# Optimization experiments

Hardware: AMD Instinct MI355X
Metric: run time of the kernel (lower is better)

Reference implementation:

```python
import jax, jax.numpy as jnp
import numpy as np

OBS_DIM = 256
FEAT = 128
HID = 64
N_OPT = 8
ACT_N = 18
B = 32768
TEMPERATURE = 1.0


def setup_inputs() -> dict:
    key = jax.random.key(0)
    ks = jax.random.split(key, 16)
    s = 0.05
    inp = {
        "obs": jax.random.normal(ks[0], (B, OBS_DIM), dtype=jnp.float32),
        "act": jax.random.randint(ks[1], (B,), 0, ACT_N, dtype=jnp.int32),
        "opt": jax.random.randint(ks[2], (B,), 0, N_OPT, dtype=jnp.int32),
        # feature trunk: obs_dim -> 64 -> 128, ReLU after both layers
        "fW1": jax.random.normal(ks[3], (HID, OBS_DIM), dtype=jnp.float32) * s,
        "fb1": jnp.zeros((HID,), dtype=jnp.float32),
        "fW2": jax.random.normal(ks[4], (FEAT, HID), dtype=jnp.float32) * s,
        "fb2": jnp.zeros((FEAT,), dtype=jnp.float32),
        # option policy / termination heads: 128 -> n_opts
        "pW": jax.random.normal(ks[5], (N_OPT, FEAT), dtype=jnp.float32) * s,
        "pb": jnp.zeros((N_OPT,), dtype=jnp.float32),
        "tW": jax.random.normal(ks[6], (N_OPT, FEAT), dtype=jnp.float32) * s,
        "tb": jnp.zeros((N_OPT,), dtype=jnp.float32),
        # per-option expert ensemble: 128 -> 64 -> act_n
        "oW1": jax.random.normal(ks[7], (N_OPT, HID, FEAT), dtype=jnp.float32) * s,
        "ob1": jnp.zeros((N_OPT, HID), dtype=jnp.float32),
        "oW2": jax.random.normal(ks[8], (N_OPT, ACT_N, HID), dtype=jnp.float32) * s,
        "ob2": jnp.zeros((N_OPT, ACT_N), dtype=jnp.float32),
    }
    return inp


def reference(obs, act, opt, fW1, fb1, fW2, fb2, pW, pb, tW, tb, oW1, ob1, oW2, ob2):
    # feature trunk (ReLU output activation as in mlp(..., output_activation=nn.ReLU))
    h = jax.nn.relu(obs @ fW1.T + fb1)          # [B, 64]
    state = jax.nn.relu(h @ fW2.T + fb2)        # [B, 128]

    # per-sample option-gathered expert MLP (vmap(fmodel) with params p[option])
    W1 = oW1[opt]                               # [B, 64, 128] irregular gather
    b1 = ob1[opt]                               # [B, 64]
    W2 = oW2[opt]                               # [B, act_n, 64]
    b2 = ob2[opt]                               # [B, act_n]
    eh = jax.nn.relu(jnp.einsum("bf,bhf->bh", state, W1) + b1)   # [B, 64]
    logits = jnp.einsum("bh,bah->ba", eh, W2) + b2               # [B, act_n]

    # Categorical(probs=softmax(logits / T)); log_prob(act) = log_softmax(logits/T)[act]
    logp_all = jax.nn.log_softmax(logits / TEMPERATURE, axis=-1)
    logp = jnp.take_along_axis(logp_all, act[:, None].astype(jnp.int32), axis=-1)[:, 0]

    # option value: take_along_dim(opt_dist, opt)
    opt_dist = state @ pW.T + pb                # [B, n_opts]
    optval = jnp.take_along_axis(opt_dist, opt[:, None].astype(jnp.int32), axis=-1)[:, 0]

    # termination prob: sigmoid(termination(state))[opt]
    term_dist = jax.nn.sigmoid(state @ tW.T + tb)
    termprob = jnp.take_along_axis(term_dist, opt[:, None].astype(jnp.int32), axis=-1)[:, 0]

    return (logp, optval, termprob)
```

## Files before the change

kernel.cpp:

```cpp
#include <hip/hip_runtime.h>
#include <hip/hip_bf16.h>
#include <math.h>

#define OBS_DIM 256
#define FEAT 128
#define HID 64
#define N_OPT 8
#define ACT_N 18
#define BATCH 32768

typedef unsigned short u16;
typedef unsigned int u32;
typedef __attribute__((ext_vector_type(8))) short short8;
typedef __attribute__((ext_vector_type(4))) float f32x4;

#define MFMA(a, b, c) __builtin_amdgcn_mfma_f32_16x16x32_bf16((a), (b), (c), 0, 0, 0)

union frag_u { u32 u[4]; short8 s; };

#define TRK_U16 28672
#define EXP_U16 81920

#define L_WB0 0
#define L_S   20480
#define L_WB1 20480
#define L_PW  49152
#define L_TW  53248
#define L_LL  49152
#define L_LH  57344
#define L_E   57344

__device__ __forceinline__ u16 bf(float x) {
    u32 u = __float_as_uint(x);
    return (u16)((u + 0x7fffu + ((u >> 16) & 1u)) >> 16);
}
__device__ __forceinline__ u32 cvtpk(float lo, float hi) {
    u32 r;
    asm("v_cvt_pk_bf16_f32 %0, %1, %2" : "=v"(r) : "v"(lo), "v"(hi));
    return r;
}

__global__ __launch_bounds__(256) void k_prep(
    const float* __restrict__ fW1, const float* __restrict__ fW2,
    const float* __restrict__ pW,  const float* __restrict__ tW,
    const float* __restrict__ oW1, const float* __restrict__ oW2,
    u16* __restrict__ dst)
{
    int gid = blockIdx.x * 256 + threadIdx.x;
    int stride = gridDim.x * 256;
    for (int i = gid; i < TRK_U16 + EXP_U16; i += stride) {
        float v;
        if (i < TRK_U16) {
            int f = i >> 9, l = (i >> 3) & 63, j = i & 7;
            int lc = l & 15, lg = l >> 4;
            if (f < 32) {
                int ks = f >> 2, nn = f & 3;
                v = fW1[(nn * 16 + lc) * 256 + ks * 32 + lg * 8 + j];
            } else if (f < 48) {
                int f2 = f - 32, ks = f2 >> 3, nn = f2 & 7;
                v = fW2[(nn * 16 + lc) * 64 + ks * 32 + lg * 8 + j];
            } else if (f < 52) {
                int ks = f - 48;
                v = (lc < N_OPT) ? pW[lc * 128 + ks * 32 + lg * 8 + j] : 0.f;
            } else {
                int ks = f - 52;
                v = (lc < N_OPT) ? tW[lc * 128 + ks * 32 + lg * 8 + j] : 0.f;
            }
        } else {
            int t = i - TRK_U16;
            int o = t / 10240, t2 = t - o * 10240;
            int f = t2 >> 9, l = (t2 >> 3) & 63, j = t2 & 7;
            int lc = l & 15, lg = l >> 4;
            if (f < 16) {
                int ks = f >> 2, nn = f & 3;
                v = oW1[o * 8192 + (nn * 16 + lc) * 128 + ks * 32 + lg * 8 + j];
            } else {
                int f2 = f - 16, ks = f2 >> 1, nn = f2 & 1;
                int row = nn * 16 + lc;
                v = (row < ACT_N) ? oW2[o * (ACT_N * 64) + row * 64 + ks * 32 + lg * 8 + j] : 0.f;
            }
        }
        dst[i] = bf(v);
    }
}

__global__ __launch_bounds__(256, 2) void k_fused(
    const float* __restrict__ obs, const int* __restrict__ opt,
    const int* __restrict__ act,
    const u16* __restrict__ trkw, const u16* __restrict__ expw,
    const float* __restrict__ fb1, const float* __restrict__ fb2,
    const float* __restrict__ pb,  const float* __restrict__ tb,
    const float* __restrict__ ob1, const float* __restrict__ ob2,
    float* __restrict__ out)
{
    __shared__ char lmem[65536];
    const int tid = threadIdx.x;
    const int tile = blockIdx.x;
    const int w = tid >> 6, l = tid & 63, lg = l >> 4, lc = l & 15;
    const int l16 = l * 16;

    const float* orow = obs + (size_t)(tile * 64 + 16 * w + lc) * OBS_DIM + lg * 8;
    float4 of[16];
#pragma unroll
    for (int ks = 0; ks < 8; ++ks) {
        of[2 * ks]     = *reinterpret_cast<const float4*>(orow + ks * 32);
        of[2 * ks + 1] = *reinterpret_cast<const float4*>(orow + ks * 32 + 4);
    }
    int ro[4];
#pragma unroll
    for (int r = 0; r < 4; ++r) ro[r] = opt[tile * 64 + 16 * w + 4 * lg + r];
    int myact = act[tile * 64 + (tid >> 2)];
    float fb1v[4], fb2v[8];
#pragma unroll
    for (int nn = 0; nn < 4; ++nn) fb1v[nn] = fb1[nn * 16 + lc];
#pragma unroll
    for (int nn = 0; nn < 8; ++nn) fb2v[nn] = fb2[nn * 16 + lc];

#pragma unroll
    for (int i = 0; i < 14; ++i) {
        int f = w * 14 + i;
        __builtin_amdgcn_global_load_lds((const void*)(trkw + f * 512 + l * 8),
                                         (void*)(lmem + f * 1024), 16, 0, 0);
    }

    frag_u a1[8];
#pragma unroll
    for (int ks = 0; ks < 8; ++ks) {
        a1[ks].u[0] = cvtpk(of[2 * ks].x,     of[2 * ks].y);
        a1[ks].u[1] = cvtpk(of[2 * ks].z,     of[2 * ks].w);
        a1[ks].u[2] = cvtpk(of[2 * ks + 1].x, of[2 * ks + 1].y);
        a1[ks].u[3] = cvtpk(of[2 * ks + 1].z, of[2 * ks + 1].w);
    }
    float pbr[4], tbr[4];
#pragma unroll
    for (int r = 0; r < 4; ++r) { pbr[r] = pb[ro[r]]; tbr[r] = tb[ro[r]]; }

    __syncthreads();

    f32x4 acc1[4] = {{0,0,0,0},{0,0,0,0},{0,0,0,0},{0,0,0,0}};
#pragma unroll
    for (int ks = 0; ks < 8; ++ks) {
#pragma unroll
        for (int nn = 0; nn < 4; ++nn) {
            short8 b = *reinterpret_cast<const short8*>(lmem + (ks * 4 + nn) * 1024 + l16);
            acc1[nn] = MFMA(a1[ks].s, b, acc1[nn]);
        }
    }
#pragma unroll
    for (int nn = 0; nn < 4; ++nn) {
#pragma unroll
        for (int r = 0; r < 4; ++r) {
            u16 hv = bf(fmaxf(acc1[nn][r] + fb1v[nn], 0.f));
            int ad = L_LH + w * 2048 + (nn >> 1) * 1024
                   + (((((nn & 1) * 2 + (lc >> 3)) * 16) + 4 * lg + r) << 4) + ((lc & 7) << 1);
            *(u16*)(lmem + ad) = hv;
        }
    }
    __syncthreads();

#pragma unroll
    for (int i = 0; i < 5; ++i) {
        int f = w * 5 + i;
        __builtin_amdgcn_global_load_lds((const void*)(expw + f * 512 + l * 8),
                                         (void*)(lmem + L_WB0 + f * 1024), 16, 0, 0);
    }

    f32x4 acc2[8];
#pragma unroll
    for (int nn = 0; nn < 8; ++nn) acc2[nn] = (f32x4){0,0,0,0};
#pragma unroll
    for (int ks = 0; ks < 2; ++ks) {
        short8 a = *reinterpret_cast<const short8*>(lmem + L_LH + w * 2048 + ks * 1024 + l16);
#pragma unroll
        for (int nn = 0; nn < 8; ++nn) {
            short8 b = *reinterpret_cast<const short8*>(lmem + (32 + ks * 8 + nn) * 1024 + l16);
            acc2[nn] = MFMA(a, b, acc2[nn]);
        }
    }
    __syncthreads();

#pragma unroll
    for (int nn = 0; nn < 8; ++nn) {
#pragma unroll
        for (int r = 0; r < 4; ++r) {
            u16 sv = bf(fmaxf(acc2[nn][r] + fb2v[nn], 0.f));
            int ad = L_S + w * 4096 + (nn >> 1) * 1024
                   + (((((nn & 1) * 2 + (lc >> 3)) * 16) + 4 * lg + r) << 4) + ((lc & 7) << 1);
            *(u16*)(lmem + ad) = sv;
        }
    }
    short8 a4[4];
#pragma unroll
    for (int ks = 0; ks < 4; ++ks)
        a4[ks] = *reinterpret_cast<const short8*>(lmem + L_S + w * 4096 + ks * 1024 + l16);

    f32x4 accP = {0,0,0,0}, accT = {0,0,0,0};
#pragma unroll
    for (int ks = 0; ks < 4; ++ks) {
        short8 bp = *reinterpret_cast<const short8*>(lmem + L_PW + ks * 1024 + l16);
        short8 bt = *reinterpret_cast<const short8*>(lmem + L_TW + ks * 1024 + l16);
        accP = MFMA(a4[ks], bp, accP);
        accT = MFMA(a4[ks], bt, accT);
    }
#pragma unroll
    for (int r = 0; r < 4; ++r) {
        int grow = tile * 64 + 16 * w + 4 * lg + r;
        float pv = __shfl(accP[r], (l & 48) | ro[r], 64);
        float tv = __shfl(accT[r], (l & 48) | ro[r], 64);
        if (lc == 0) {
            out[BATCH + grow] = pv + pbr[r];
            out[2 * BATCH + grow] = 1.f / (1.f + expf(-(tv + tbr[r])));
        }
    }
    __syncthreads();

#pragma unroll
    for (int i = 0; i < 5; ++i) {
        int f = w * 5 + i;
        __builtin_amdgcn_global_load_lds((const void*)(expw + 10240 + f * 512 + l * 8),
                                         (void*)(lmem + L_WB1 + f * 1024), 16, 0, 0);
    }

    float* lL = (float*)(lmem + L_LL);
#pragma unroll
    for (int o = 0; o < N_OPT; ++o) {
        const char* wb = lmem + ((o & 1) ? L_WB1 : L_WB0);

        f32x4 acc[4] = {{0,0,0,0},{0,0,0,0},{0,0,0,0},{0,0,0,0}};
#pragma unroll
        for (int ks = 0; ks < 4; ++ks) {
#pragma unroll
            for (int nn = 0; nn < 4; ++nn) {
                short8 b = *reinterpret_cast<const short8*>(wb + (ks * 4 + nn) * 1024 + l16);
                acc[nn] = MFMA(a4[ks], b, acc[nn]);
            }
        }
#pragma unroll
        for (int nn = 0; nn < 4; ++nn) {
            float bias = ob1[o * HID + nn * 16 + lc];
#pragma unroll
            for (int r = 0; r < 4; ++r) {
                if (ro[r] == o) {
                    u16 ev = bf(fmaxf(acc[nn][r] + bias, 0.f));
                    int ad = L_E + w * 2048 + (nn >> 1) * 1024
                           + (((((nn & 1) * 2 + (lc >> 3)) * 16) + 4 * lg + r) << 4) + ((lc & 7) << 1);
                    *(u16*)(lmem + ad) = ev;
                }
            }
        }
        short8 a2[2];
#pragma unroll
        for (int ks = 0; ks < 2; ++ks)
            a2[ks] = *reinterpret_cast<const short8*>(lmem + L_E + w * 2048 + ks * 1024 + l16);
        f32x4 accl[2] = {{0,0,0,0},{0,0,0,0}};
#pragma unroll
        for (int ks = 0; ks < 2; ++ks) {
#pragma unroll
            for (int nn = 0; nn < 2; ++nn) {
                short8 b = *reinterpret_cast<const short8*>(wb + (16 + ks * 2 + nn) * 1024 + l16);
                accl[nn] = MFMA(a2[ks], b, accl[nn]);
            }
        }
#pragma unroll
        for (int nn = 0; nn < 2; ++nn) {
            int col = nn * 16 + lc;
            if (col < ACT_N) {
                float bias = ob2[o * ACT_N + col];
#pragma unroll
                for (int r = 0; r < 4; ++r)
                    if (ro[r] == o) lL[(16 * w + 4 * lg + r) * 19 + col] = accl[nn][r] + bias;
            }
        }
        __syncthreads();
        if (o < 6) {
            char* db = lmem + ((o & 1) ? L_WB1 : L_WB0);
#pragma unroll
            for (int i = 0; i < 5; ++i) {
                int f = w * 5 + i;
                __builtin_amdgcn_global_load_lds((const void*)(expw + (o + 2) * 10240 + f * 512 + l * 8),
                                                 (void*)(db + f * 1024), 16, 0, 0);
            }
        }
    }

    {
        int row = tid >> 2, q = tid & 3;
        const float* lr = lL + row * 19;
        float mx = -1e30f;
        for (int a = q; a < ACT_N; a += 4) mx = fmaxf(mx, lr[a]);
        mx = fmaxf(mx, __shfl_xor(mx, 1, 64));
        mx = fmaxf(mx, __shfl_xor(mx, 2, 64));
        float s = 0.f;
        for (int a = q; a < ACT_N; a += 4) s += expf(lr[a] - mx);
        s += __shfl_xor(s, 1, 64);
        s += __shfl_xor(s, 2, 64);
        if (q == 0) out[tile * 64 + row] = (lr[myact] - mx) - logf(s);
    }
}

extern "C" void kernel_launch(void* const* d_in, const int* in_sizes, int n_in,
                              void* d_out, int out_size, void* d_ws, size_t ws_size,
                              hipStream_t stream) {
    const float* obs = (const float*)d_in[0];
    const int*   act = (const int*)d_in[1];
    const int*   opt = (const int*)d_in[2];
    const float* fW1 = (const float*)d_in[3];
    const float* fb1 = (const float*)d_in[4];
    const float* fW2 = (const float*)d_in[5];
    const float* fb2 = (const float*)d_in[6];
    const float* pW  = (const float*)d_in[7];
    const float* pb  = (const float*)d_in[8];
    const float* tW  = (const float*)d_in[9];
    const float* tb  = (const float*)d_in[10];
    const float* oW1 = (const float*)d_in[11];
    const float* ob1 = (const float*)d_in[12];
    const float* oW2 = (const float*)d_in[13];
    const float* ob2 = (const float*)d_in[14];
    float* out = (float*)d_out;

    u16* wsu = (u16*)d_ws;
    const u16* trkw = wsu;
    const u16* expw = wsu + TRK_U16;

    k_prep<<<64, 256, 0, stream>>>(fW1, fW2, pW, tW, oW1, oW2, wsu);
    k_fused<<<BATCH / 64, 256, 0, stream>>>(obs, opt, act, trkw, expw,
                                            fb1, fb2, pb, tb, ob1, ob2, out);
}
```

Measured before the change: 119.5 us.

## Shrink LDS arena and stage trunk weights in halves for three blocks per CU

```diff
diff --git a/kernel.cpp b/kernel.cpp
--- a/kernel.cpp
+++ b/kernel.cpp
@@ -21,14 +21,13 @@
 #define TRK_U16 28672
 #define EXP_U16 81920
 
+#define L_LH  32768
+#define L_LS  16384
 #define L_WB0 0
-#define L_S   20480
 #define L_WB1 20480
-#define L_PW  49152
-#define L_TW  53248
+#define L_E   40960
 #define L_LL  49152
-#define L_LH  57344
-#define L_E   57344
+#define ARENA 54016
 
 __device__ __forceinline__ u16 bf(float x) {
     u32 u = __float_as_uint(x);
@@ -84,7 +83,7 @@
     }
 }
 
-__global__ __launch_bounds__(256, 2) void k_fused(
+__global__ __launch_bounds__(256, 3) void k_fused(
     const float* __restrict__ obs, const int* __restrict__ opt,
     const int* __restrict__ act,
     const u16* __restrict__ trkw, const u16* __restrict__ expw,
@@ -93,53 +92,89 @@
     const float* __restrict__ ob1, const float* __restrict__ ob2,
     float* __restrict__ out)
 {
-    __shared__ char lmem[65536];
+    __shared__ char lmem[ARENA];
     const int tid = threadIdx.x;
     const int tile = blockIdx.x;
     const int w = tid >> 6, l = tid & 63, lg = l >> 4, lc = l & 15;
     const int l16 = l * 16;
 
+#pragma unroll
+    for (int i = 0; i < 8; ++i) {
+        int f = w * 8 + i;
+        __builtin_amdgcn_global_load_lds((const void*)(trkw + f * 512 + l * 8),
+                                         (void*)(lmem + f * 1024), 16, 0, 0);
+    }
+
     const float* orow = obs + (size_t)(tile * 64 + 16 * w + lc) * OBS_DIM + lg * 8;
-    float4 of[16];
-#pragma unroll
-    for (int ks = 0; ks < 8; ++ks) {
-        of[2 * ks]     = *reinterpret_cast<const float4*>(orow + ks * 32);
-        of[2 * ks + 1] = *reinterpret_cast<const float4*>(orow + ks * 32 + 4);
+    frag_u a1[8];
+    {
+        float4 of[8];
+#pragma unroll
+        for (int ks = 0; ks < 4; ++ks) {
+            of[2 * ks]     = *reinterpret_cast<const float4*>(orow + ks * 32);
+            of[2 * ks + 1] = *reinterpret_cast<const float4*>(orow + ks * 32 + 4);
+        }
+#pragma unroll
+        for (int ks = 0; ks < 4; ++ks) {
+            a1[ks].u[0] = cvtpk(of[2 * ks].x,     of[2 * ks].y);
+            a1[ks].u[1] = cvtpk(of[2 * ks].z,     of[2 * ks].w);
+            a1[ks].u[2] = cvtpk(of[2 * ks + 1].x, of[2 * ks + 1].y);
+            a1[ks].u[3] = cvtpk(of[2 * ks + 1].z, of[2 * ks + 1].w);
+        }
+#pragma unroll
+        for (int ks = 4; ks < 8; ++ks) {
+            of[2 * (ks - 4)]     = *reinterpret_cast<const float4*>(orow + ks * 32);
+            of[2 * (ks - 4) + 1] = *reinterpret_cast<const float4*>(orow + ks * 32 + 4);
+        }
+#pragma unroll
+        for (int ks = 4; ks < 8; ++ks) {
+            a1[ks].u[0] = cvtpk(of[2 * (ks - 4)].x,     of[2 * (ks - 4)].y);
+            a1[ks].u[1] = cvtpk(of[2 * (ks - 4)].z,     of[2 * (ks - 4)].w);
+            a1[ks].u[2] = cvtpk(of[2 * (ks - 4) + 1].x, of[2 * (ks - 4) + 1].y);
+            a1[ks].u[3] = cvtpk(of[2 * (ks - 4) + 1].z, of[2 * (ks - 4) + 1].w);
+        }
     }
     int ro[4];
 #pragma unroll
     for (int r = 0; r < 4; ++r) ro[r] = opt[tile * 64 + 16 * w + 4 * lg + r];
     int myact = act[tile * 64 + (tid >> 2)];
+    float pbr[4], tbr[4];
+#pragma unroll
+    for (int r = 0; r < 4; ++r) { pbr[r] = pb[ro[r]]; tbr[r] = tb[ro[r]]; }
     float fb1v[4], fb2v[8];
 #pragma unroll
     for (int nn = 0; nn < 4; ++nn) fb1v[nn] = fb1[nn * 16 + lc];
 #pragma unroll
     for (int nn = 0; nn < 8; ++nn) fb2v[nn] = fb2[nn * 16 + lc];
 
-#pragma unroll
-    for (int i = 0; i < 14; ++i) {
-        int f = w * 14 + i;
-        __builtin_amdgcn_global_load_lds((const void*)(trkw + f * 512 + l * 8),
+    __syncthreads();
+
+    f32x4 acc1[4] = {{0,0,0,0},{0,0,0,0},{0,0,0,0},{0,0,0,0}};
+#pragma unroll
+    for (int ks = 0; ks < 4; ++ks) {
+#pragma unroll
+        for (int nn = 0; nn < 4; ++nn) {
+            short8 b = *reinterpret_cast<const short8*>(lmem + (ks * 4 + nn) * 1024 + l16);
+            acc1[nn] = MFMA(a1[ks].s, b, acc1[nn]);
+        }
+    }
+    __syncthreads();
+
+#pragma unroll
+    for (int i = 0; i < 4; ++i) {
+        int f = w * 4 + i;
+        __builtin_amdgcn_global_load_lds((const void*)(trkw + (32 + f) * 512 + l * 8),
                                          (void*)(lmem + f * 1024), 16, 0, 0);
     }
-
-    frag_u a1[8];
-#pragma unroll
-    for (int ks = 0; ks < 8; ++ks) {
-        a1[ks].u[0] = cvtpk(of[2 * ks].x,     of[2 * ks].y);
-        a1[ks].u[1] = cvtpk(of[2 * ks].z,     of[2 * ks].w);
-        a1[ks].u[2] = cvtpk(of[2 * ks + 1].x, of[2 * ks + 1].y);
-        a1[ks].u[3] = cvtpk(of[2 * ks + 1].z, of[2 * ks + 1].w);
-    }
-    float pbr[4], tbr[4];
-#pragma unroll
-    for (int r = 0; r < 4; ++r) { pbr[r] = pb[ro[r]]; tbr[r] = tb[ro[r]]; }
-
-    __syncthreads();
-
-    f32x4 acc1[4] = {{0,0,0,0},{0,0,0,0},{0,0,0,0},{0,0,0,0}};
-#pragma unroll
-    for (int ks = 0; ks < 8; ++ks) {
+    short8 bpr[4], btr[4];
+#pragma unroll
+    for (int ks = 0; ks < 4; ++ks) {
+        bpr[ks] = *reinterpret_cast<const short8*>(trkw + (48 + ks) * 512 + l * 8);
+        btr[ks] = *reinterpret_cast<const short8*>(trkw + (52 + ks) * 512 + l * 8);
+    }
+
+#pragma unroll
+    for (int ks = 4; ks < 8; ++ks) {
 #pragma unroll
         for (int nn = 0; nn < 4; ++nn) {
             short8 b = *reinterpret_cast<const short8*>(lmem + (ks * 4 + nn) * 1024 + l16);
@@ -158,68 +193,64 @@
     }
     __syncthreads();
 
+    f32x4 acc2[8];
+#pragma unroll
+    for (int nn = 0; nn < 8; ++nn) acc2[nn] = (f32x4){0,0,0,0};
+#pragma unroll
+    for (int ks = 0; ks < 2; ++ks) {
+        short8 a = *reinterpret_cast<const short8*>(lmem + L_LH + w * 2048 + ks * 1024 + l16);
+#pragma unroll
+        for (int nn = 0; nn < 8; ++nn) {
+            short8 b = *reinterpret_cast<const short8*>(lmem + (ks * 8 + nn) * 1024 + l16);
+            acc2[nn] = MFMA(a, b, acc2[nn]);
+        }
+    }
+
+#pragma unroll
+    for (int nn = 0; nn < 8; ++nn) {
+#pragma unroll
+        for (int r = 0; r < 4; ++r) {
+            u16 sv = bf(fmaxf(acc2[nn][r] + fb2v[nn], 0.f));
+            int ad = L_LS + w * 4096 + (nn >> 1) * 1024
+                   + (((((nn & 1) * 2 + (lc >> 3)) * 16) + 4 * lg + r) << 4) + ((lc & 7) << 1);
+            *(u16*)(lmem + ad) = sv;
+        }
+    }
+    short8 a4[4];
+#pragma unroll
+    for (int ks = 0; ks < 4; ++ks)
+        a4[ks] = *reinterpret_cast<const short8*>(lmem + L_LS + w * 4096 + ks * 1024 + l16);
+
+    __syncthreads();
+
 #pragma unroll
     for (int i = 0; i < 5; ++i) {
         int f = w * 5 + i;
         __builtin_amdgcn_global_load_lds((const void*)(expw + f * 512 + l * 8),
                                          (void*)(lmem + L_WB0 + f * 1024), 16, 0, 0);
-    }
-
-    f32x4 acc2[8];
-#pragma unroll
-    for (int nn = 0; nn < 8; ++nn) acc2[nn] = (f32x4){0,0,0,0};
-#pragma unroll
-    for (int ks = 0; ks < 2; ++ks) {
-        short8 a = *reinterpret_cast<const short8*>(lmem + L_LH + w * 2048 + ks * 1024 + l16);
-#pragma unroll
-        for (int nn = 0; nn < 8; ++nn) {
-            short8 b = *reinterpret_cast<const short8*>(lmem + (32 + ks * 8 + nn) * 1024 + l16);
-            acc2[nn] = MFMA(a, b, acc2[nn]);
-        }
-    }
-    __syncthreads();
-
-#pragma unroll
-    for (int nn = 0; nn < 8; ++nn) {
-#pragma unroll
-        for (int r = 0; r < 4; ++r) {
-            u16 sv = bf(fmaxf(acc2[nn][r] + fb2v[nn], 0.f));
-            int ad = L_S + w * 4096 + (nn >> 1) * 1024
-                   + (((((nn & 1) * 2 + (lc >> 3)) * 16) + 4 * lg + r) << 4) + ((lc & 7) << 1);
-            *(u16*)(lmem + ad) = sv;
-        }
-    }
-    short8 a4[4];
-#pragma unroll
-    for (int ks = 0; ks < 4; ++ks)
-        a4[ks] = *reinterpret_cast<const short8*>(lmem + L_S + w * 4096 + ks * 1024 + l16);
-
-    f32x4 accP = {0,0,0,0}, accT = {0,0,0,0};
-#pragma unroll
-    for (int ks = 0; ks < 4; ++ks) {
-        short8 bp = *reinterpret_cast<const short8*>(lmem + L_PW + ks * 1024 + l16);
-        short8 bt = *reinterpret_cast<const short8*>(lmem + L_TW + ks * 1024 + l16);
-        accP = MFMA(a4[ks], bp, accP);
-        accT = MFMA(a4[ks], bt, accT);
-    }
-#pragma unroll
-    for (int r = 0; r < 4; ++r) {
-        int grow = tile * 64 + 16 * w + 4 * lg + r;
-        float pv = __shfl(accP[r], (l & 48) | ro[r], 64);
-        float tv = __shfl(accT[r], (l & 48) | ro[r], 64);
-        if (lc == 0) {
-            out[BATCH + grow] = pv + pbr[r];
-            out[2 * BATCH + grow] = 1.f / (1.f + expf(-(tv + tbr[r])));
-        }
-    }
-    __syncthreads();
-
-#pragma unroll
-    for (int i = 0; i < 5; ++i) {
-        int f = w * 5 + i;
         __builtin_amdgcn_global_load_lds((const void*)(expw + 10240 + f * 512 + l * 8),
                                          (void*)(lmem + L_WB1 + f * 1024), 16, 0, 0);
     }
+
+    {
+        f32x4 accP = {0,0,0,0}, accT = {0,0,0,0};
+#pragma unroll
+        for (int ks = 0; ks < 4; ++ks) {
+            accP = MFMA(a4[ks], bpr[ks], accP);
+            accT = MFMA(a4[ks], btr[ks], accT);
+        }
+#pragma unroll
+        for (int r = 0; r < 4; ++r) {
+            int grow = tile * 64 + 16 * w + 4 * lg + r;
+            float pv = __shfl(accP[r], (l & 48) | ro[r], 64);
+            float tv = __shfl(accT[r], (l & 48) | ro[r], 64);
+            if (lc == 0) {
+                out[BATCH + grow] = pv + pbr[r];
+                out[2 * BATCH + grow] = 1.f / (1.f + expf(-(tv + tbr[r])));
+            }
+        }
+    }
+    __syncthreads();
 
     float* lL = (float*)(lmem + L_LL);
 #pragma unroll
@@ -271,14 +302,17 @@
                     if (ro[r] == o) lL[(16 * w + 4 * lg + r) * 19 + col] = accl[nn][r] + bias;
             }
         }
-        __syncthreads();
-        if (o < 6) {
-            char* db = lmem + ((o & 1) ? L_WB1 : L_WB0);
-#pragma unroll
-            for (int i = 0; i < 5; ++i) {
-                int f = w * 5 + i;
-                __builtin_amdgcn_global_load_lds((const void*)(expw + (o + 2) * 10240 + f * 512 + l * 8),
-                                                 (void*)(db + f * 1024), 16, 0, 0);
+        if (o < 7) {
+            __syncthreads();
+            if (o < 6) {
+                char* db = lmem + ((o & 1) ? L_WB1 : L_WB0);
+#pragma unroll
+                for (int i = 0; i < 5; ++i) {
+                    int f = w * 5 + i;
+                    __builtin_amdgcn_global_load_lds(
+                        (const void*)(expw + (o + 2) * 10240 + f * 512 + l * 8),
+                        (void*)(db + f * 1024), 16, 0, 0);
+                }
             }
         }
     }
```

Result: no change. 118.3 us (-1.0%).
